# Performance work log

Measured on AMD Instinct MI355X. Metric: run time of the kernel, lower is better.

The kernel has to match this reference:

```python
import jax, jax.numpy as jnp
import numpy as np

D_MODEL = 1024
NUM_HEADS = 16
D_K = D_MODEL // NUM_HEADS
NEG = -1e9


def setup_inputs() -> dict:
    key = jax.random.key(0)
    ks = jax.random.split(key, 7)
    B, S = 2, 2048
    q = jax.random.normal(ks[0], (B, S, D_MODEL), dtype=jnp.float32)
    k = jax.random.normal(ks[1], (B, S, D_MODEL), dtype=jnp.float32)
    v = jax.random.normal(ks[2], (B, S, D_MODEL), dtype=jnp.float32)
    mask = jnp.ones((B, S), dtype=jnp.int32)
    # nn.Linear(d_model, d_model, bias=False): y = x @ W.T, W:[out,in]
    scale = 1.0 / np.sqrt(D_MODEL)
    Wq = jax.random.normal(ks[3], (D_MODEL, D_MODEL), dtype=jnp.float32) * scale
    Wk = jax.random.normal(ks[4], (D_MODEL, D_MODEL), dtype=jnp.float32) * scale
    Wv = jax.random.normal(ks[5], (D_MODEL, D_MODEL), dtype=jnp.float32) * scale
    Wo = jax.random.normal(ks[6], (D_MODEL, D_MODEL), dtype=jnp.float32) * scale
    return {"q": q, "k": k, "v": v, "mask": mask,
            "Wq": Wq, "Wk": Wk, "Wv": Wv, "Wo": Wo}


def _split_heads(x, B):
    # [B,S,D] -> [B,H,S,d_k]
    return x.reshape(B, -1, NUM_HEADS, D_K).transpose(0, 2, 1, 3)


def reference(q, k, v, mask, Wq, Wk, Wv, Wo):
    B = q.shape[0]
    qh = _split_heads(q @ Wq.T, B)
    kh = _split_heads(k @ Wk.T, B)
    vh = _split_heads(v @ Wv.T, B)
    # [B,H,Sq,Sk]
    scores = jnp.einsum('bhqd,bhkd->bhqk', qh, kh) / jnp.sqrt(jnp.float32(D_K))
    Sq, Sk = scores.shape[-2], scores.shape[-1]
    causal = jnp.triu(jnp.ones((Sq, Sk), dtype=bool), k=1)
    scores = jnp.where(causal[None, None], NEG, scores)
    pad = (mask[:, None, None, :] == 0)  # [B,1,1,Sk]
    scores = jnp.where(pad, NEG, scores)
    weights = jax.nn.softmax(scores, axis=-1)
    out = jnp.einsum('bhqk,bhkd->bhqd', weights, vh)
    out = out.transpose(0, 2, 1, 3).reshape(B, -1, D_MODEL)
    return out @ Wo.T
```

## Files before the change

### kernel.cpp

```cpp
#include <hip/hip_runtime.h>
#include <hip/hip_bf16.h>
#include <stdint.h>

using bf16 = __hip_bfloat16;
typedef __attribute__((ext_vector_type(8))) short short8;
typedef __attribute__((ext_vector_type(4))) float f32x4;
typedef __attribute__((ext_vector_type(16))) float f32x16;
typedef __attribute__((ext_vector_type(4))) float float4v;
typedef __attribute__((ext_vector_type(4))) unsigned short us4;
typedef __attribute__((ext_vector_type(4))) uint32_t u32x4;

#define LDS_U32 __attribute__((address_space(3))) uint32_t
#define GLB_U32 __attribute__((address_space(1))) uint32_t

__device__ __forceinline__ unsigned short f2b(float f) {
  union { float f; uint32_t u; } x; x.f = f;
  uint32_t r = x.u + 0x7FFFu + ((x.u >> 16) & 1u);
  return (unsigned short)(r >> 16);
}

__device__ __forceinline__ void stage8(const float* __restrict__ src, bf16* dst) {
  float4v x0 = *(const float4v*)src;
  float4v x1 = *(const float4v*)(src + 4);
  uint32_t p0, p1, p2, p3;
  asm("v_cvt_pk_bf16_f32 %0, %1, %2" : "=v"(p0) : "v"(x0.x), "v"(x0.y));
  asm("v_cvt_pk_bf16_f32 %0, %1, %2" : "=v"(p1) : "v"(x0.z), "v"(x0.w));
  asm("v_cvt_pk_bf16_f32 %0, %1, %2" : "=v"(p2) : "v"(x1.x), "v"(x1.y));
  asm("v_cvt_pk_bf16_f32 %0, %1, %2" : "=v"(p3) : "v"(x1.z), "v"(x1.w));
  u32x4 w = {p0, p1, p2, p3};
  *(u32x4*)dst = w;
}

__global__ __launch_bounds__(256, 2)
void qkv_proj(const float* __restrict__ Aq, const float* __restrict__ Ak,
              const float* __restrict__ Av,
              const float* __restrict__ Wq, const float* __restrict__ Wk,
              const float* __restrict__ Wv,
              bf16* __restrict__ Qh, bf16* __restrict__ KF, bf16* __restrict__ VF) {
  __shared__ bf16 Alds[128 * 64];
  __shared__ bf16 Blds[128 * 64];
  const int t = threadIdx.x, lane = t & 63, wave = t >> 6;
  const int l15 = lane & 15, l4 = lane >> 4;
  const int seg = blockIdx.x >> 3;
  const int n0 = (blockIdx.x & 7) * 128;
  const int m0 = blockIdx.y * 128;
  const float* A = (seg == 0) ? Aq : (seg == 1) ? Ak : Av;
  const float* B = (seg == 0) ? Wq : (seg == 1) ? Wk : Wv;
  const int K = 1024;
  const int wr = (wave >> 1) * 64, wc = (wave & 1) * 64;
  const float SCLE = 0.18033688011112042f;

  f32x4 acc[4][4] = {};

  for (int kt = 0; kt < K; kt += 64) {
#pragma unroll
    for (int i = 0; i < 4; ++i) {
      int f = i * 256 + t, row = f >> 3, cc = f & 7, ch = cc ^ (row & 7);
      stage8(A + (size_t)(m0 + row) * K + kt + cc * 8, Alds + row * 64 + ch * 8);
      stage8(B + (size_t)(n0 + row) * K + kt + cc * 8, Blds + row * 64 + ch * 8);
    }
    __syncthreads();
#pragma unroll
    for (int ks = 0; ks < 2; ++ks) {
      short8 af[4], bfr[4];
#pragma unroll
      for (int mi = 0; mi < 4; ++mi) {
        int row = wr + mi * 16 + l15;
        int ch = (ks * 4 + l4) ^ (row & 7);
        af[mi] = *(const short8*)(Alds + row * 64 + ch * 8);
      }
#pragma unroll
      for (int ni = 0; ni < 4; ++ni) {
        int row = wc + ni * 16 + l15;
        int ch = (ks * 4 + l4) ^ (row & 7);
        bfr[ni] = *(const short8*)(Blds + row * 64 + ch * 8);
      }
#pragma unroll
      for (int mi = 0; mi < 4; ++mi)
#pragma unroll
        for (int ni = 0; ni < 4; ++ni)
          acc[mi][ni] = __builtin_amdgcn_mfma_f32_16x16x32_bf16(
              af[mi], bfr[ni], acc[mi][ni], 0, 0, 0);
    }
    __syncthreads();
  }

#pragma unroll
  for (int mi = 0; mi < 4; ++mi) {
#pragma unroll
    for (int ni = 0; ni < 4; ++ni) {
      int rbase = m0 + wr + mi * 16 + l4 * 4;
      int col = n0 + wc + ni * 16 + l15;
      if (seg == 0) {
        unsigned short* C = (unsigned short*)Qh;
#pragma unroll
        for (int r = 0; r < 4; ++r)
          C[(size_t)(rbase + r) * 1024 + col] = f2b(acc[mi][ni][r] * SCLE);
      } else if (seg == 1) {
        unsigned short* C = (unsigned short*)KF;
        int h = col >> 6, d = col & 63;
#pragma unroll
        for (int r = 0; r < 4; ++r) {
          int row = rbase + r;
          int b = row >> 11, s = row & 2047;
          size_t idx = (size_t)(b * 16 + h) * 131072 +
                       ((((s >> 5) * 4 + (d >> 4)) * 2 + ((d >> 3) & 1)) * 256) +
                       (s & 31) * 8 + (d & 7);
          C[idx] = f2b(acc[mi][ni][r]);
        }
      } else {
        unsigned short* C = (unsigned short*)VF;
        int h = col >> 6, d = col & 63;
        int row = rbase;
        int b = row >> 11, s = row & 2047;
        size_t idx = (size_t)(b * 16 + h) * 131072 +
                     (((((s >> 6) * 2 + ((d >> 5) & 1)) * 4 + ((s >> 4) & 3)) * 2 +
                       ((s >> 3) & 1)) * 256) +
                     (d & 31) * 8 + (s & 7);
        us4 y;
        y.x = f2b(acc[mi][ni][0]); y.y = f2b(acc[mi][ni][1]);
        y.z = f2b(acc[mi][ni][2]); y.w = f2b(acc[mi][ni][3]);
        *(us4*)(C + idx) = y;
      }
    }
  }
}

__global__ __launch_bounds__(256, 2)
void gemm_o(const bf16* __restrict__ A, const float* __restrict__ B,
            float* __restrict__ C) {
  __shared__ bf16 Alds[128 * 64];
  __shared__ bf16 Blds[64 * 64];
  const int t = threadIdx.x, lane = t & 63, wave = t >> 6;
  const int l15 = lane & 15, l4 = lane >> 4;
  const int n0 = blockIdx.x * 64, m0 = blockIdx.y * 128;
  const int K = 1024;
  const int wr = (wave >> 1) * 64, wc = (wave & 1) * 32;

  f32x4 acc[4][2] = {};

  for (int kt = 0; kt < K; kt += 64) {
#pragma unroll
    for (int i = 0; i < 4; ++i) {
      int f = i * 256 + t, row = f >> 3, csrc = (f & 7) ^ (row & 7);
      __builtin_amdgcn_global_load_lds(
          (const GLB_U32*)(A + (size_t)(m0 + row) * K + kt + csrc * 8),
          (LDS_U32*)(Alds + f * 8), 16, 0, 0);
    }
#pragma unroll
    for (int i = 0; i < 2; ++i) {
      int f = i * 256 + t, row = f >> 3, cc = f & 7, ch = cc ^ (row & 7);
      stage8(B + (size_t)(n0 + row) * K + kt + cc * 8, Blds + row * 64 + ch * 8);
    }
    __syncthreads();
#pragma unroll
    for (int ks = 0; ks < 2; ++ks) {
      short8 af[4], bfr[2];
#pragma unroll
      for (int mi = 0; mi < 4; ++mi) {
        int row = wr + mi * 16 + l15;
        int ch = (ks * 4 + l4) ^ (row & 7);
        af[mi] = *(const short8*)(Alds + row * 64 + ch * 8);
      }
#pragma unroll
      for (int ni = 0; ni < 2; ++ni) {
        int row = wc + ni * 16 + l15;
        int ch = (ks * 4 + l4) ^ (row & 7);
        bfr[ni] = *(const short8*)(Blds + row * 64 + ch * 8);
      }
#pragma unroll
      for (int mi = 0; mi < 4; ++mi)
#pragma unroll
        for (int ni = 0; ni < 2; ++ni)
          acc[mi][ni] = __builtin_amdgcn_mfma_f32_16x16x32_bf16(
              af[mi], bfr[ni], acc[mi][ni], 0, 0, 0);
    }
    __syncthreads();
  }

#pragma unroll
  for (int mi = 0; mi < 4; ++mi)
#pragma unroll
    for (int ni = 0; ni < 2; ++ni) {
      int rbase = m0 + wr + mi * 16 + l4 * 4;
      int col = n0 + wc + ni * 16 + l15;
#pragma unroll
      for (int r = 0; r < 4; ++r)
        C[(size_t)(rbase + r) * 1024 + col] = acc[mi][ni][r];
    }
}

__global__ __launch_bounds__(256, 2)
void attn_fwd(const bf16* __restrict__ Q, const bf16* __restrict__ KF,
              const bf16* __restrict__ VF, const int* __restrict__ mask,
              bf16* __restrict__ O) {
  const int lin = blockIdx.x;
  const int xcd = lin & 7, q8 = lin >> 3;
  const int bh = xcd + 8 * (q8 & 3), g = q8 >> 2;
  const int b = bh >> 4, h = bh & 15;
  const int wave = threadIdx.x >> 6, lane = threadIdx.x & 63;
  const int l31 = lane & 31, hi = lane >> 5;
  const int job = 2 * g + (wave >> 1);
  const int halfk = wave & 1, wp = wave >> 1;

  __shared__ float accL[2][64][33];
  __shared__ float mlL[2][64][2];

  const size_t bqk = (size_t)b * 2048 * 1024 + h * 64;
  const size_t fbase = (size_t)bh * 131072;

  for (int si = 0; si < 2; ++si) {
    const int s = si ? (63 - job) : job;
    const int q0 = 32 * s;
    const int T = (s >> 1) + 1;
    const int hsplit = (T + 1) >> 1;
    const int tstart = halfk ? hsplit : 0;
    const int tend = halfk ? T : hsplit;

    short8 qf[4];
#pragma unroll
    for (int s4 = 0; s4 < 4; ++s4)
      qf[s4] = *(const short8*)(Q + bqk + (size_t)(q0 + l31) * 1024 + 16 * s4 + 8 * hi);

    int anyz = 0;
    for (int i = tstart * 64 + lane; i < tend * 64; i += 64)
      anyz |= (mask[b * 2048 + i] == 0);
    const bool doMask = __any(anyz);

    f32x16 acc0 = {}, acc1 = {};
    float m = -1e30f, l = 0.f;

    short8 kf[2][4], kn[2][4], vf[2][4];
    if (tstart < tend) {
#pragma unroll
      for (int u = 0; u < 2; ++u)
#pragma unroll
        for (int s4 = 0; s4 < 4; ++s4)
          kf[u][s4] = *(const short8*)(KF + fbase +
              ((size_t)((2 * tstart + u) * 4 + s4) * 2 + hi) * 256 + l31 * 8);
    }

    for (int tt = tstart; tt < tend; ++tt) {
#pragma unroll
      for (int n = 0; n < 2; ++n)
#pragma unroll
        for (int tq = 0; tq < 4; ++tq)
          vf[n][tq] = *(const short8*)(VF + fbase +
              ((size_t)(((tt * 2 + n) * 4 + tq) * 2 + hi)) * 256 + l31 * 8);

      f32x16 s0 = {}, s1 = {};
      __builtin_amdgcn_s_setprio(1);
#pragma unroll
      for (int s4 = 0; s4 < 4; ++s4) {
        s0 = __builtin_amdgcn_mfma_f32_32x32x16_bf16(kf[0][s4], qf[s4], s0, 0, 0, 0);
        s1 = __builtin_amdgcn_mfma_f32_32x32x16_bf16(kf[1][s4], qf[s4], s1, 0, 0, 0);
      }
      __builtin_amdgcn_s_setprio(0);
      if (tt + 1 < tend) {
#pragma unroll
        for (int u = 0; u < 2; ++u)
#pragma unroll
          for (int s4 = 0; s4 < 4; ++s4)
            kn[u][s4] = *(const short8*)(KF + fbase +
                ((size_t)((2 * (tt + 1) + u) * 4 + s4) * 2 + hi) * 256 + l31 * 8);
      }

      float w[2][16];
#pragma unroll
      for (int p = 0; p < 16; ++p) { w[0][p] = s0[p]; w[1][p] = s1[p]; }

      if (doMask) {
        int mv = mask[b * 2048 + tt * 64 + lane];
        uint64_t bits = __ballot(mv != 0);
        uint64_t bs = bits >> (4 * hi);
#pragma unroll
        for (int u = 0; u < 2; ++u)
#pragma unroll
          for (int p = 0; p < 16; ++p)
            if (!((bs >> (32 * u + (p & 3) + 8 * (p >> 2))) & 1)) w[u][p] = -3e38f;
      }
      if (tt == T - 1) {
        int qr = 32 * (s & 1) + l31 - 4 * hi;
#pragma unroll
        for (int u = 0; u < 2; ++u)
#pragma unroll
          for (int p = 0; p < 16; ++p)
            if (32 * u + (p & 3) + 8 * (p >> 2) > qr) w[u][p] = -3e38f;
      }

      float tm = fmaxf(w[0][0], w[1][0]);
#pragma unroll
      for (int p = 1; p < 16; ++p) tm = fmaxf(tm, fmaxf(w[0][p], w[1][p]));
      tm = fmaxf(tm, __shfl_xor(tm, 32));

      if (!__all(tm <= m + 8.f)) {
        float mn = fmaxf(m, tm);
        float corr = __builtin_amdgcn_exp2f(m - mn);
        m = mn; l *= corr;
#pragma unroll
        for (int p = 0; p < 16; ++p) {
          float ct = __shfl(corr, (p & 3) + 8 * (p >> 2) + 4 * hi);
          acc0[p] *= ct; acc1[p] *= ct;
        }
      }

      float ts = 0.f;
#pragma unroll
      for (int u = 0; u < 2; ++u)
#pragma unroll
        for (int p = 0; p < 16; ++p) {
          float pv = __builtin_amdgcn_exp2f(w[u][p] - m);
          w[u][p] = pv; ts += pv;
        }
      ts += __shfl_xor(ts, 32);
      l += ts;

      uint32_t pkk[2][8];
#pragma unroll
      for (int u = 0; u < 2; ++u)
#pragma unroll
        for (int a = 0; a < 4; ++a)
#pragma unroll
          for (int w2 = 0; w2 < 2; ++w2) {
            uint32_t r;
            asm("v_cvt_pk_bf16_f32 %0, %1, %2"
                : "=v"(r) : "v"(w[u][4 * a + 2 * w2]), "v"(w[u][4 * a + 2 * w2 + 1]));
            pkk[u][2 * a + w2] = r;
          }

#pragma unroll
      for (int tq = 0; tq < 4; ++tq) {
        const int u = tq >> 1, alo = 2 * (tq & 1);
        uint32_t a0 = pkk[u][2 * alo + 0], b0 = pkk[u][2 * alo + 2];
        uint32_t a1 = pkk[u][2 * alo + 1], b1 = pkk[u][2 * alo + 3];
        asm("v_permlane32_swap_b32 %0, %1" : "+v"(a0), "+v"(b0));
        asm("v_permlane32_swap_b32 %0, %1" : "+v"(a1), "+v"(b1));
        u32x4 wv = {a0, a1, b0, b1};
        short8 paf = __builtin_bit_cast(short8, wv);
        __builtin_amdgcn_s_setprio(1);
        acc0 = __builtin_amdgcn_mfma_f32_32x32x16_bf16(paf, vf[0][tq], acc0, 0, 0, 0);
        acc1 = __builtin_amdgcn_mfma_f32_32x32x16_bf16(paf, vf[1][tq], acc1, 0, 0, 0);
        __builtin_amdgcn_s_setprio(0);
      }

#pragma unroll
      for (int u = 0; u < 2; ++u)
#pragma unroll
        for (int s4 = 0; s4 < 4; ++s4) kf[u][s4] = kn[u][s4];
    }

    if (halfk) {
#pragma unroll
      for (int p = 0; p < 16; ++p) {
        accL[wp][lane][p] = acc0[p];
        accL[wp][lane][16 + p] = acc1[p];
      }
      mlL[wp][lane][0] = m; mlL[wp][lane][1] = l;
    }
    __syncthreads();
    if (!halfk) {
      float mB = mlL[wp][lane][0], lB = mlL[wp][lane][1];
      float ms = fmaxf(m, mB);
      float cAr = __builtin_amdgcn_exp2f(m - ms);
      float cBr = __builtin_amdgcn_exp2f(mB - ms);
      float inv = 1.f / (cAr * l + cBr * lB);
      float fa = cAr * inv, fb = cBr * inv;
      unsigned short* Ou = (unsigned short*)O;
#pragma unroll
      for (int p = 0; p < 16; ++p) {
        int crow = (p & 3) + 8 * (p >> 2) + 4 * hi;
        float faT = __shfl(fa, crow);
        float fbT = __shfl(fb, crow);
        float o0 = acc0[p] * faT + accL[wp][lane][p] * fbT;
        float o1 = acc1[p] * faT + accL[wp][lane][16 + p] * fbT;
        size_t ro = (size_t)(b * 2048 + q0 + crow) * 1024 + h * 64;
        Ou[ro + l31] = f2b(o0);
        Ou[ro + 32 + l31] = f2b(o1);
      }
    }
    __syncthreads();
  }
}

extern "C" void kernel_launch(void* const* d_in, const int* in_sizes, int n_in,
                              void* d_out, int out_size, void* d_ws, size_t ws_size,
                              hipStream_t stream) {
  const float* q = (const float*)d_in[0];
  const float* k = (const float*)d_in[1];
  const float* v = (const float*)d_in[2];
  const int* mask = (const int*)d_in[3];
  const float* Wq = (const float*)d_in[4];
  const float* Wk = (const float*)d_in[5];
  const float* Wv = (const float*)d_in[6];
  const float* Wo = (const float*)d_in[7];
  float* out = (float*)d_out;

  const size_t NT = 4096 * 1024;
  bf16* p = (bf16*)d_ws;
  bf16* Qh = p; p += NT;
  bf16* KF = p; p += NT;
  bf16* VF = p; p += NT;
  bf16* Oh = p; p += NT;

  qkv_proj<<<dim3(24, 32), 256, 0, stream>>>(q, k, v, Wq, Wk, Wv, Qh, KF, VF);
  attn_fwd<<<512, 256, 0, stream>>>(Qh, KF, VF, mask, Oh);
  gemm_o<<<dim3(16, 32), 256, 0, stream>>>(Oh, Wo, out);
}
```

Before: 223.9 us.

## Pre-cast inputs and weights to bf16, use direct global-to-LDS loads in GEMMs

Adds a separate cast kernel that converts the q/k/v activations and all four weight matrices from fp32 to bf16 once per call. Both GEMM kernels then stage their tiles with global_load_lds DMA instead of register-based fp32 load and convert. This removes the repeated fp32 reads and conversions each tile performs. Block indices are also remapped so that blocks launched together, presumably sharing an XCD, work on nearby tiles. The cost is an extra kernel launch and an extra round trip of roughly 28 MB through memory for the casts.

```diff
diff --git a/kernel.cpp b/kernel.cpp
--- a/kernel.cpp
+++ b/kernel.cpp
@@ -9,6 +9,7 @@
 typedef __attribute__((ext_vector_type(4))) float float4v;
 typedef __attribute__((ext_vector_type(4))) unsigned short us4;
 typedef __attribute__((ext_vector_type(4))) uint32_t u32x4;
+typedef __attribute__((ext_vector_type(2))) uint32_t u32x2;
 
 #define LDS_U32 __attribute__((address_space(3))) uint32_t
 #define GLB_U32 __attribute__((address_space(1))) uint32_t
@@ -19,33 +20,55 @@
   return (unsigned short)(r >> 16);
 }
 
-__device__ __forceinline__ void stage8(const float* __restrict__ src, bf16* dst) {
-  float4v x0 = *(const float4v*)src;
-  float4v x1 = *(const float4v*)(src + 4);
-  uint32_t p0, p1, p2, p3;
-  asm("v_cvt_pk_bf16_f32 %0, %1, %2" : "=v"(p0) : "v"(x0.x), "v"(x0.y));
-  asm("v_cvt_pk_bf16_f32 %0, %1, %2" : "=v"(p1) : "v"(x0.z), "v"(x0.w));
-  asm("v_cvt_pk_bf16_f32 %0, %1, %2" : "=v"(p2) : "v"(x1.x), "v"(x1.y));
-  asm("v_cvt_pk_bf16_f32 %0, %1, %2" : "=v"(p3) : "v"(x1.z), "v"(x1.w));
-  u32x4 w = {p0, p1, p2, p3};
-  *(u32x4*)dst = w;
+__global__ void cast_all(const float* __restrict__ q, const float* __restrict__ k,
+                         const float* __restrict__ v, const float* __restrict__ Wq,
+                         const float* __restrict__ Wk, const float* __restrict__ Wv,
+                         const float* __restrict__ Wo,
+                         bf16* __restrict__ qb, bf16* __restrict__ kb,
+                         bf16* __restrict__ vb, bf16* __restrict__ Wqb,
+                         bf16* __restrict__ Wkb, bf16* __restrict__ Wvb,
+                         bf16* __restrict__ Wob) {
+  const int NQ = 1 << 20;
+  const int NW = 1 << 18;
+  const int total = 3 * NQ + 4 * NW;
+  for (int i = blockIdx.x * blockDim.x + threadIdx.x; i < total;
+       i += gridDim.x * blockDim.x) {
+    const float* s; bf16* d; int vi;
+    if (i < 3 * NQ) {
+      int a = i >> 20; vi = i & (NQ - 1);
+      s = (a == 0) ? q : (a == 1) ? k : v;
+      d = (a == 0) ? qb : (a == 1) ? kb : vb;
+    } else {
+      int j = i - 3 * NQ;
+      int a = j >> 18; vi = j & (NW - 1);
+      s = (a == 0) ? Wq : (a == 1) ? Wk : (a == 2) ? Wv : Wo;
+      d = (a == 0) ? Wqb : (a == 1) ? Wkb : (a == 2) ? Wvb : Wob;
+    }
+    float4v x = ((const float4v*)s)[vi];
+    us4 y;
+    y.x = f2b(x.x); y.y = f2b(x.y); y.z = f2b(x.z); y.w = f2b(x.w);
+    ((us4*)d)[vi] = y;
+  }
 }
 
 __global__ __launch_bounds__(256, 2)
-void qkv_proj(const float* __restrict__ Aq, const float* __restrict__ Ak,
-              const float* __restrict__ Av,
-              const float* __restrict__ Wq, const float* __restrict__ Wk,
-              const float* __restrict__ Wv,
+void qkv_proj(const bf16* __restrict__ Aq, const bf16* __restrict__ Ak,
+              const bf16* __restrict__ Av,
+              const bf16* __restrict__ Wq, const bf16* __restrict__ Wk,
+              const bf16* __restrict__ Wv,
               bf16* __restrict__ Qh, bf16* __restrict__ KF, bf16* __restrict__ VF) {
   __shared__ bf16 Alds[128 * 64];
   __shared__ bf16 Blds[128 * 64];
   const int t = threadIdx.x, lane = t & 63, wave = t >> 6;
   const int l15 = lane & 15, l4 = lane >> 4;
-  const int seg = blockIdx.x >> 3;
-  const int n0 = (blockIdx.x & 7) * 128;
-  const int m0 = blockIdx.y * 128;
-  const float* A = (seg == 0) ? Aq : (seg == 1) ? Ak : Av;
-  const float* B = (seg == 0) ? Wq : (seg == 1) ? Wk : Wv;
+  const int p = blockIdx.x;
+  const int l = (p & 7) * 96 + (p >> 3);
+  const int grp = l >> 3;
+  const int n0 = (l & 7) * 128;
+  const int seg = grp >> 5;
+  const int m0 = (grp & 31) * 128;
+  const bf16* A = (seg == 0) ? Aq : (seg == 1) ? Ak : Av;
+  const bf16* B = (seg == 0) ? Wq : (seg == 1) ? Wk : Wv;
   const int K = 1024;
   const int wr = (wave >> 1) * 64, wc = (wave & 1) * 64;
   const float SCLE = 0.18033688011112042f;
@@ -55,9 +78,13 @@
   for (int kt = 0; kt < K; kt += 64) {
 #pragma unroll
     for (int i = 0; i < 4; ++i) {
-      int f = i * 256 + t, row = f >> 3, cc = f & 7, ch = cc ^ (row & 7);
-      stage8(A + (size_t)(m0 + row) * K + kt + cc * 8, Alds + row * 64 + ch * 8);
-      stage8(B + (size_t)(n0 + row) * K + kt + cc * 8, Blds + row * 64 + ch * 8);
+      int f = i * 256 + t, row = f >> 3, csrc = (f & 7) ^ (row & 7);
+      __builtin_amdgcn_global_load_lds(
+          (const GLB_U32*)(A + (size_t)(m0 + row) * K + kt + csrc * 8),
+          (LDS_U32*)(Alds + f * 8), 16, 0, 0);
+      __builtin_amdgcn_global_load_lds(
+          (const GLB_U32*)(B + (size_t)(n0 + row) * K + kt + csrc * 8),
+          (LDS_U32*)(Blds + f * 8), 16, 0, 0);
     }
     __syncthreads();
 #pragma unroll
@@ -127,13 +154,16 @@
 }
 
 __global__ __launch_bounds__(256, 2)
-void gemm_o(const bf16* __restrict__ A, const float* __restrict__ B,
+void gemm_o(const bf16* __restrict__ A, const bf16* __restrict__ B,
             float* __restrict__ C) {
   __shared__ bf16 Alds[128 * 64];
   __shared__ bf16 Blds[64 * 64];
   const int t = threadIdx.x, lane = t & 63, wave = t >> 6;
   const int l15 = lane & 15, l4 = lane >> 4;
-  const int n0 = blockIdx.x * 64, m0 = blockIdx.y * 128;
+  const int p = blockIdx.x;
+  const int l = (p & 7) * 64 + (p >> 3);
+  const int m0 = (l >> 4) * 128;
+  const int n0 = (l & 15) * 64;
   const int K = 1024;
   const int wr = (wave >> 1) * 64, wc = (wave & 1) * 32;
 
@@ -149,8 +179,10 @@
     }
 #pragma unroll
     for (int i = 0; i < 2; ++i) {
-      int f = i * 256 + t, row = f >> 3, cc = f & 7, ch = cc ^ (row & 7);
-      stage8(B + (size_t)(n0 + row) * K + kt + cc * 8, Blds + row * 64 + ch * 8);
+      int f = i * 256 + t, row = f >> 3, csrc = (f & 7) ^ (row & 7);
+      __builtin_amdgcn_global_load_lds(
+          (const GLB_U32*)(B + (size_t)(n0 + row) * K + kt + csrc * 8),
+          (LDS_U32*)(Blds + f * 8), 16, 0, 0);
     }
     __syncthreads();
 #pragma unroll
@@ -396,13 +428,23 @@
   float* out = (float*)d_out;
 
   const size_t NT = 4096 * 1024;
+  const size_t NW = 1024 * 1024;
   bf16* p = (bf16*)d_ws;
-  bf16* Qh = p; p += NT;
-  bf16* KF = p; p += NT;
-  bf16* VF = p; p += NT;
-  bf16* Oh = p; p += NT;
-
-  qkv_proj<<<dim3(24, 32), 256, 0, stream>>>(q, k, v, Wq, Wk, Wv, Qh, KF, VF);
+  bf16* qb = p;  p += NT;
+  bf16* kb = p;  p += NT;
+  bf16* vb = p;  p += NT;
+  bf16* Wqb = p; p += NW;
+  bf16* Wkb = p; p += NW;
+  bf16* Wvb = p; p += NW;
+  bf16* Wob = p; p += NW;
+  bf16* Qh = p;  p += NT;
+  bf16* KF = p;  p += NT;
+  bf16* VF = p;  p += NT;
+  bf16* Oh = p;  p += NT;
+
+  cast_all<<<2048, 256, 0, stream>>>(q, k, v, Wq, Wk, Wv, Wo,
+                                     qb, kb, vb, Wqb, Wkb, Wvb, Wob);
+  qkv_proj<<<768, 256, 0, stream>>>(qb, kb, vb, Wqb, Wkb, Wvb, Qh, KF, VF);
   attn_fwd<<<512, 256, 0, stream>>>(Qh, KF, VF, mask, Oh);
-  gemm_o<<<dim3(16, 32), 256, 0, stream>>>(Oh, Wo, out);
-}
+  gemm_o<<<512, 256, 0, stream>>>(Oh, Wob, out);
+}
```

Measured after the change: 201.7 us. 9.9% less time.
